# Optimization experiments

Hardware: AMD Instinct MI355X
Metric: run time of the kernel (lower is better)

Reference implementation:

```python
import jax, jax.numpy as jnp
import numpy as np

B, S, D = 4, 2048, 1024

def setup_inputs() -> dict:
    key = jax.random.key(0)
    k0, k1, k2, k3 = jax.random.split(key, 4)
    scale = 1.0 / np.sqrt(D)
    return {
        "x": jax.random.normal(k0, (B, S, D), dtype=jnp.float32),
        "Wq": jax.random.normal(k1, (D, D), dtype=jnp.float32) * scale,
        "Wk": jax.random.normal(k2, (D, D), dtype=jnp.float32) * scale,
        "Wv": jax.random.normal(k3, (D, D), dtype=jnp.float32) * scale,
    }

def reference(x, Wq, Wk, Wv):
    # x: [B,S,D]; Wq/Wk/Wv: [D_in, D_out] (equivalent to torch Linear weight transposed)
    q = jnp.einsum('bsd,de->bse', x, Wq)
    k = jnp.einsum('bsd,de->bse', x, Wk)
    v = jnp.einsum('bsd,de->bse', x, Wv)
    d_out = k.shape[-1]
    scores = jnp.einsum('bqe,bke->bqk', q, k)  # [B,S,S]
    S_ = scores.shape[-1]
    causal = jnp.tril(jnp.ones((S_, S_), dtype=bool))  # True = keep
    # masked_fill before scaling == after scaling (-inf invariant under positive scale)
    scores = jnp.where(causal, scores, -jnp.inf)
    attn = jax.nn.softmax(scores / jnp.sqrt(jnp.asarray(d_out, scores.dtype)), axis=-1)
    # dropout p=0.0 -> identity
    return jnp.einsum('bqk,bke->bqe', attn, v)
```

## Files before the change

kernel.cpp:

```cpp
#include <hip/hip_runtime.h>

#define B_  4
#define S_  2048
#define D_  1024
#define N_  (B_*S_)
#define SCALE 0.03125f
#define NEGINF (-3.0e38f)

typedef unsigned short u16;
typedef __attribute__((ext_vector_type(8))) short short8;
typedef __attribute__((ext_vector_type(4))) float floatx4;

__device__ __forceinline__ u16 f2bf(float f) {
    unsigned int u = __float_as_uint(f);
    u += 0x7FFFu + ((u >> 16) & 1u);
    return (u16)(u >> 16);
}
__device__ __forceinline__ float bf2f(u16 h) {
    return __uint_as_float((unsigned int)h << 16);
}

__device__ __forceinline__ void gl_lds16(const void* g, void* l) {
    __builtin_amdgcn_global_load_lds(
        (const __attribute__((address_space(1))) unsigned int*)g,
        (__attribute__((address_space(3))) unsigned int*)l, 16, 0, 0);
}

__device__ __forceinline__ int xcd_chunk(int bid, int nwg) {
    return (bid & 7) * (nwg >> 3) + (bid >> 3);
}

__global__ __launch_bounds__(256) void cast_fused(const float* __restrict__ x,
                                                  const float* __restrict__ Wq, const float* __restrict__ Wk,
                                                  const float* __restrict__ Wv,
                                                  u16* __restrict__ xb, u16* __restrict__ Wqb,
                                                  u16* __restrict__ Wkb, u16* __restrict__ Wvt) {
    __shared__ float t[32][33];
    const int blk = blockIdx.x;
    if (blk < 5120) {
        const float* src; u16* dst; size_t i;
        if (blk < 4096)      { src = x;  dst = xb;  i = (size_t)blk * 2048; }
        else if (blk < 4608) { src = Wq; dst = Wqb; i = (size_t)(blk - 4096) * 2048; }
        else                 { src = Wk; dst = Wkb; i = (size_t)(blk - 4608) * 2048; }
        i += (size_t)threadIdx.x * 8;
        float4 a = *(const float4*)&src[i];
        float4 b = *(const float4*)&src[i + 4];
        short8 o;
        o[0]=f2bf(a.x); o[1]=f2bf(a.y); o[2]=f2bf(a.z); o[3]=f2bf(a.w);
        o[4]=f2bf(b.x); o[5]=f2bf(b.y); o[6]=f2bf(b.z); o[7]=f2bf(b.w);
        *(short8*)&dst[i] = o;
    } else {
        const int tb = blk - 5120;
        const int c = threadIdx.x & 31, r0 = threadIdx.x >> 5;
        const int i0 = (tb >> 5) * 32, j0 = (tb & 31) * 32;
#pragma unroll
        for (int rr = 0; rr < 4; ++rr)
            t[r0 + rr * 8][c] = Wv[(size_t)(i0 + r0 + rr * 8) * D_ + j0 + c];
        __syncthreads();
#pragma unroll
        for (int rr = 0; rr < 4; ++rr)
            Wvt[(size_t)(j0 + r0 + rr * 8) * D_ + i0 + c] = f2bf(t[c][r0 + rr * 8]);
    }
}

__device__ __forceinline__ void mfma_nt_loop(const u16* __restrict__ A, int lda,
                                             const u16* __restrict__ Bp, int ldb,
                                             int m0, int n0, int kext,
                                             u16* As, u16* Bs, floatx4 acc[4][4])
{
    const int tid  = threadIdx.x;
    const int lane = tid & 63;
    const int lr   = lane & 15, quad = lane >> 4;
    const int wm   = ((tid >> 6) & 1) * 64, wn = (tid >> 7) * 64;
    const int e    = tid * 8;
    const int nt   = kext >> 6;

    auto stage = [&](int k0, int half) {
        u16* Ad = As + half * 8192;
        u16* Bd = Bs + half * 8192;
#pragma unroll
        for (int it = 0; it < 4; ++it) {
            int idx = it * 2048 + e;
            int row = idx >> 6;
            int cg  = (idx & 63) >> 3;
            int gc  = (cg ^ (row & 7)) << 3;
            gl_lds16(&A [(size_t)(m0 + row) * lda + k0 + gc], &Ad[idx]);
            gl_lds16(&Bp[(size_t)(n0 + row) * ldb + k0 + gc], &Bd[idx]);
        }
    };

    stage(0, 0);
    int cur = 0;
    for (int t = 0; t < nt; ++t) {
        if (t + 1 < nt) {
            stage((t + 1) << 6, cur ^ 1);
            asm volatile("s_waitcnt vmcnt(8)" ::: "memory");
        } else {
            asm volatile("s_waitcnt vmcnt(0)" ::: "memory");
        }
        __builtin_amdgcn_s_barrier();

        const u16* Asb = As + cur * 8192;
        const u16* Bsb = Bs + cur * 8192;
#pragma unroll
        for (int kk = 0; kk < 2; ++kk) {
            short8 af[4], bf[4];
            const int kg = kk * 4 + quad;
#pragma unroll
            for (int i = 0; i < 4; ++i) {
                int am = wm + i * 16 + lr;
                af[i] = *(const short8*)&Asb[am * 64 + ((kg ^ (am & 7)) << 3)];
                int bn = wn + i * 16 + lr;
                bf[i] = *(const short8*)&Bsb[bn * 64 + ((kg ^ (bn & 7)) << 3)];
            }
            __builtin_amdgcn_s_setprio(1);
#pragma unroll
            for (int i = 0; i < 4; ++i)
#pragma unroll
                for (int j = 0; j < 4; ++j)
                    acc[i][j] = __builtin_amdgcn_mfma_f32_16x16x32_bf16(af[i], bf[j], acc[i][j], 0, 0, 0);
            __builtin_amdgcn_s_setprio(0);
        }
        asm volatile("s_waitcnt lgkmcnt(0)" ::: "memory");
        __builtin_amdgcn_s_barrier();
        cur ^= 1;
    }
}

#define EPI_VARS                                              \
    const int lane = threadIdx.x & 63;                        \
    const int lr = lane & 15, quad = lane >> 4;               \
    const int wm = ((threadIdx.x >> 6) & 1) * 64, wn = (threadIdx.x >> 7) * 64;

__device__ __forceinline__ void mfma_nt_256(const u16* __restrict__ A, int lda,
                                            const u16* __restrict__ Bp, int ldb,
                                            int m0, int n0, int kext,
                                            u16* As, u16* Bs, floatx4 acc[8][4])
{
    const int tid  = threadIdx.x;
    const int lane = tid & 63;
    const int lr   = lane & 15, quad = lane >> 4;
    const int wid  = tid >> 6;
    const int wr   = wid >> 2;
    const int wc   = wid & 3;
    const int nt   = kext >> 6;

    auto stage2 = [&](int t, int c0) {
        const int k0 = t << 6;
        u16* Ad = As + (t & 1) * 16384;
        u16* Bd = Bs + (t & 1) * 16384;
#pragma unroll
        for (int c = c0; c < c0 + 2; ++c) {
            int idx = (c & 3) * 4096 + tid * 8;
            int row = idx >> 6;
            int cg  = (idx & 63) >> 3;
            int gc  = (cg ^ (row & 7)) << 3;
            if (c < 4) gl_lds16(&A [(size_t)(m0 + row) * lda + k0 + gc], &Ad[idx]);
            else       gl_lds16(&Bp[(size_t)(n0 + row) * ldb + k0 + gc], &Bd[idx]);
        }
    };

    stage2(0, 0); stage2(0, 2); stage2(0, 4); stage2(0, 6);

    for (int t = 0; t < nt; ++t) {
        const u16* Asb = As + (t & 1) * 16384;
        const u16* Bsb = Bs + (t & 1) * 16384;
        const bool pf = (t + 1 < nt);

        short8 af[4][2], bfA[2][2], bfB[2][2];

#pragma unroll
        for (int p = 0; p < 4; ++p) {
            if (p == 0) {
                if (pf) { stage2(t + 1, 0);
                          asm volatile("s_waitcnt vmcnt(2)" ::: "memory"); }
                else      asm volatile("s_waitcnt vmcnt(0)" ::: "memory");
                __builtin_amdgcn_s_barrier();
            } else if (pf) {
                stage2(t + 1, p * 2);
            }

            if (p == 0) {
#pragma unroll
                for (int i = 0; i < 4; ++i) {
                    int am = wr * 128 + i * 16 + lr;
#pragma unroll
                    for (int kk = 0; kk < 2; ++kk)
                        af[i][kk] = *(const short8*)&Asb[am * 64 + (((kk * 4 + quad) ^ (am & 7)) << 3)];
                }
#pragma unroll
                for (int j = 0; j < 2; ++j) {
                    int bn = wc * 64 + j * 16 + lr;
#pragma unroll
                    for (int kk = 0; kk < 2; ++kk)
                        bfA[j][kk] = *(const short8*)&Bsb[bn * 64 + (((kk * 4 + quad) ^ (bn & 7)) << 3)];
                }
            } else if (p == 1) {
#pragma unroll
                for (int j = 0; j < 2; ++j) {
                    int bn = wc * 64 + (j + 2) * 16 + lr;
#pragma unroll
                    for (int kk = 0; kk < 2; ++kk)
                        bfB[j][kk] = *(const short8*)&Bsb[bn * 64 + (((kk * 4 + quad) ^ (bn & 7)) << 3)];
                }
            } else if (p == 2) {
#pragma unroll
                for (int i = 0; i < 4; ++i) {
                    int am = wr * 128 + (i + 4) * 16 + lr;
#pragma unroll
                    for (int kk = 0; kk < 2; ++kk)
                        af[i][kk] = *(const short8*)&Asb[am * 64 + (((kk * 4 + quad) ^ (am & 7)) << 3)];
                }
            }

            const int mb = (p >> 1) * 4, nb = (p & 1) * 2;
            __builtin_amdgcn_s_setprio(1);
#pragma unroll
            for (int kk = 0; kk < 2; ++kk)
#pragma unroll
                for (int i = 0; i < 4; ++i)
#pragma unroll
                    for (int j = 0; j < 2; ++j)
                        acc[mb + i][nb + j] = __builtin_amdgcn_mfma_f32_16x16x32_bf16(
                            af[i][kk], (p & 1) ? bfB[j][kk] : bfA[j][kk], acc[mb + i][nb + j], 0, 0, 0);
            __builtin_amdgcn_s_setprio(0);
            asm volatile("s_waitcnt lgkmcnt(0)" ::: "memory");
            __builtin_amdgcn_s_barrier();
        }
    }
}

#define EPI256_VARS                                           \
    const int lane = threadIdx.x & 63;                        \
    const int lr = lane & 15, quad = lane >> 4;               \
    const int wr = (threadIdx.x >> 8) & 1, wc = (threadIdx.x >> 6) & 3;

__global__ __launch_bounds__(256) void mt_mfma(const u16* __restrict__ Wkb, const u16* __restrict__ Wqb,
                                               u16* __restrict__ Mt)
{
    __shared__ u16 As[16384], Bs[16384];
    const int m0 = blockIdx.y * 128, n0 = blockIdx.x * 128;
    floatx4 acc[4][4];
#pragma unroll
    for (int i = 0; i < 4; ++i)
#pragma unroll
        for (int j = 0; j < 4; ++j) acc[i][j] = (floatx4){0.f, 0.f, 0.f, 0.f};
    mfma_nt_loop(Wkb, D_, Wqb, D_, m0, n0, D_, As, Bs, acc);

    EPI_VARS
#pragma unroll
    for (int i = 0; i < 4; ++i)
#pragma unroll
        for (int j = 0; j < 4; ++j)
#pragma unroll
            for (int r = 0; r < 4; ++r)
                Mt[(size_t)(m0 + wm + i * 16 + quad * 4 + r) * D_ + n0 + wn + j * 16 + lr] = f2bf(acc[i][j][r]);
}

__global__ __launch_bounds__(512, 2) void yv_mfma(const u16* __restrict__ xb, const u16* __restrict__ Mt,
                                                  const u16* __restrict__ Wvt,
                                                  u16* __restrict__ Y, u16* __restrict__ Vt)
{
    __shared__ u16 As[32768], Bs[32768];
    const int lid = xcd_chunk(blockIdx.x, 256);
    floatx4 acc[8][4];
#pragma unroll
    for (int i = 0; i < 8; ++i)
#pragma unroll
        for (int j = 0; j < 4; ++j) acc[i][j] = (floatx4){0.f, 0.f, 0.f, 0.f};

    if (lid < 128) {
        const int m0 = (lid >> 2) * 256, n0 = (lid & 3) * 256;
        mfma_nt_256(xb, D_, Mt, D_, m0, n0, D_, As, Bs, acc);
        EPI256_VARS
#pragma unroll
        for (int i = 0; i < 8; ++i)
#pragma unroll
            for (int j = 0; j < 4; ++j)
#pragma unroll
                for (int r = 0; r < 4; ++r)
                    Y[(size_t)(m0 + wr * 128 + i * 16 + quad * 4 + r) * D_ + n0 + wc * 64 + j * 16 + lr]
                        = f2bf(acc[i][j][r]);
    } else {
        const int v = lid - 128;
        const int b = v >> 5;
        const int mloc = ((v >> 2) & 7) * 256;
        const int n0 = (v & 3) * 256;
        const int m0 = b * S_ + mloc;
        u16* Vb = Vt + (size_t)b * D_ * S_;
        mfma_nt_256(xb, D_, Wvt, D_, m0, n0, D_, As, Bs, acc);
        EPI256_VARS
#pragma unroll
        for (int i = 0; i < 8; ++i)
#pragma unroll
            for (int j = 0; j < 4; ++j) {
                const int ee = n0 + wc * 64 + j * 16 + lr;
                const int s4 = mloc + wr * 128 + i * 16 + quad * 4;
                ushort4 o;
                o.x = f2bf(acc[i][j][0]); o.y = f2bf(acc[i][j][1]);
                o.z = f2bf(acc[i][j][2]); o.w = f2bf(acc[i][j][3]);
                *(ushort4*)&Vb[(size_t)ee * S_ + s4] = o;
            }
    }
}

__global__ __launch_bounds__(512, 2) void scores_mfma(const u16* __restrict__ Y, const u16* __restrict__ xb,
                                                      u16* __restrict__ Sc)
{
    __shared__ u16 As[32768], Bs[32768];
    const int lid = xcd_chunk(blockIdx.x, 144);
    const int b = lid / 36;
    const int t = lid - b * 36;
    int qt = 0;
    while ((qt + 1) * (qt + 2) / 2 <= t) ++qt;
    const int kt = t - qt * (qt + 1) / 2;

    const u16* A  = Y  + (size_t)b * S_ * D_;
    const u16* Bp = xb + (size_t)b * S_ * D_;
    u16* Sb = Sc + (size_t)b * S_ * S_;
    const int m0 = qt * 256, n0 = kt * 256;
    floatx4 acc[8][4];
#pragma unroll
    for (int i = 0; i < 8; ++i)
#pragma unroll
        for (int j = 0; j < 4; ++j) acc[i][j] = (floatx4){0.f, 0.f, 0.f, 0.f};
    mfma_nt_256(A, D_, Bp, D_, m0, n0, D_, As, Bs, acc);

    EPI256_VARS
#pragma unroll
    for (int i = 0; i < 8; ++i)
#pragma unroll
        for (int r = 0; r < 4; ++r) {
            const int grow = m0 + wr * 128 + i * 16 + quad * 4 + r;
#pragma unroll
            for (int j = 0; j < 4; ++j) {
                const int gcol = n0 + wc * 64 + j * 16 + lr;
                const float v = (gcol <= grow) ? acc[i][j][r] * SCALE : NEGINF;
                Sb[(size_t)grow * S_ + gcol] = f2bf(v);
            }
        }
}

__global__ __launch_bounds__(256) void softmax_k(const u16* __restrict__ Sc, u16* __restrict__ P)
{
    const int row = blockIdx.x;
    const int b = row >> 11, q = row & (S_ - 1);
    const int L = ((q >> 7) + 1) << 7;
    const u16* rp = Sc + ((size_t)b * S_ + q) * S_;
    u16* pp = P + ((size_t)b * S_ + q) * S_;
    __shared__ float red[4];
    __shared__ float bc;
    const int tid = threadIdx.x;
    const int i = tid << 3;
    const bool act = i < L;

    float f[8];
    float lmax = -3.4e38f;
    if (act) {
        short8 v = *(const short8*)&rp[i];
#pragma unroll
        for (int k = 0; k < 8; ++k) { f[k] = bf2f((u16)v[k]); lmax = fmaxf(lmax, f[k]); }
    }
    for (int off = 32; off; off >>= 1) lmax = fmaxf(lmax, __shfl_down(lmax, off, 64));
    if ((tid & 63) == 0) red[tid >> 6] = lmax;
    __syncthreads();
    if (tid == 0) bc = fmaxf(fmaxf(red[0], red[1]), fmaxf(red[2], red[3]));
    __syncthreads();
    const float m = bc;

    float lsum = 0.f;
    if (act) {
#pragma unroll
        for (int k = 0; k < 8; ++k) { f[k] = __expf(f[k] - m); lsum += f[k]; }
    }
    for (int off = 32; off; off >>= 1) lsum += __shfl_down(lsum, off, 64);
    if ((tid & 63) == 0) red[tid >> 6] = lsum;
    __syncthreads();
    if (tid == 0) bc = red[0] + red[1] + red[2] + red[3];
    __syncthreads();
    const float inv = 1.0f / bc;

    if (act) {
        short8 o;
#pragma unroll
        for (int k = 0; k < 8; ++k) o[k] = (short)f2bf(f[k] * inv);
        *(short8*)&pp[i] = o;
    }
}

__global__ __launch_bounds__(256) void pv_mfma(const u16* __restrict__ P, const u16* __restrict__ Vt,
                                               float* __restrict__ O)
{
    const int lid = xcd_chunk(blockIdx.x, 512);
    const int b  = lid >> 7;
    const int r  = lid & 127;
    const int et = r >> 4, qt = r & 15;
    __shared__ u16 As[16384], Bs[16384];
    const u16* A  = P  + (size_t)b * S_ * S_;
    const u16* Bp = Vt + (size_t)b * D_ * S_;
    const int m0 = qt * 128, n0 = et * 128;
    const int kext = (qt + 1) * 128;
    floatx4 acc[4][4];
#pragma unroll
    for (int i = 0; i < 4; ++i)
#pragma unroll
        for (int j = 0; j < 4; ++j) acc[i][j] = (floatx4){0.f, 0.f, 0.f, 0.f};
    mfma_nt_loop(A, S_, Bp, S_, m0, n0, kext, As, Bs, acc);

    EPI_VARS
#pragma unroll
    for (int i = 0; i < 4; ++i)
#pragma unroll
        for (int r2 = 0; r2 < 4; ++r2) {
            const int grow = m0 + wm + i * 16 + quad * 4 + r2;
#pragma unroll
            for (int j = 0; j < 4; ++j)
                O[((size_t)b * S_ + grow) * D_ + n0 + wn + j * 16 + lr] = acc[i][j][r2];
        }
}

extern "C" void kernel_launch(void* const* d_in, const int* in_sizes, int n_in,
                              void* d_out, int out_size, void* d_ws, size_t ws_size,
                              hipStream_t stream) {
    const float* x  = (const float*)d_in[0];
    const float* Wq = (const float*)d_in[1];
    const float* Wk = (const float*)d_in[2];
    const float* Wv = (const float*)d_in[3];
    float* out = (float*)d_out;
    char* w = (char*)d_ws;

    u16* xb  = (u16*)(w);
    u16* Wqb = (u16*)(w + 16777216);
    u16* Wkb = (u16*)(w + 18874368);
    u16* Wvt = (u16*)(w + 20971520);
    u16* Mt  = (u16*)(w + 23068672);
    u16* Y   = (u16*)(w + 25165824);
    u16* Vt  = (u16*)(w + 41943040);
    u16* Sc  = (u16*)(w + 58720256);
    u16* P   = (u16*)(w + 92274688);

    cast_fused <<<dim3(6144),   256, 0, stream>>>(x, Wq, Wk, Wv, xb, Wqb, Wkb, Wvt);
    mt_mfma    <<<dim3(8, 8),   256, 0, stream>>>(Wkb, Wqb, Mt);
    yv_mfma    <<<dim3(256),    512, 0, stream>>>(xb, Mt, Wvt, Y, Vt);
    scores_mfma<<<dim3(144),    512, 0, stream>>>(Y, xb, Sc);
    softmax_k  <<<dim3(N_),     256, 0, stream>>>(Sc, P);
    pv_mfma    <<<dim3(512),    256, 0, stream>>>(P, Vt, out);
}
```

Measured before the change: 233.9 us.

## Restructure MFMA GEMM LDS layout into k-half slabs with finer-grained prefetch pipelining

Both the 128- and 256-tile NT GEMM mainloops now store LDS tiles as separate 32-wide k-half slabs with a 4-way XOR swizzle, in one unified shared buffer. Global-to-LDS prefetch of the next tile is split into smaller chunks interleaved between MFMA phases, with adjusted vmcnt waits. In the 256 kernel the wave mapping changes and B fragments are reused across two M halves, cutting LDS reads. The goal is better overlap of loads with MFMA and fewer bank conflicts, at the cost of more barriers per k-step.

Result: faster. 226.5 us (-3.2%).

```diff
diff --git a/kernel.cpp b/kernel.cpp
--- a/kernel.cpp
+++ b/kernel.cpp
@@ -63,56 +63,58 @@
     }
 }
 
-__device__ __forceinline__ void mfma_nt_loop(const u16* __restrict__ A, int lda,
-                                             const u16* __restrict__ Bp, int ldb,
-                                             int m0, int n0, int kext,
-                                             u16* As, u16* Bs, floatx4 acc[4][4])
+
+__device__ __forceinline__ void mfma_nt_128(const u16* __restrict__ A, int lda,
+                                            const u16* __restrict__ Bp, int ldb,
+                                            int m0, int n0, int kext,
+                                            u16* Sh, floatx4 acc[4][4])
 {
     const int tid  = threadIdx.x;
     const int lane = tid & 63;
     const int lr   = lane & 15, quad = lane >> 4;
     const int wm   = ((tid >> 6) & 1) * 64, wn = (tid >> 7) * 64;
-    const int e    = tid * 8;
     const int nt   = kext >> 6;
 
-    auto stage = [&](int k0, int half) {
-        u16* Ad = As + half * 8192;
-        u16* Bd = Bs + half * 8192;
-#pragma unroll
-        for (int it = 0; it < 4; ++it) {
-            int idx = it * 2048 + e;
-            int row = idx >> 6;
-            int cg  = (idx & 63) >> 3;
-            int gc  = (cg ^ (row & 7)) << 3;
-            gl_lds16(&A [(size_t)(m0 + row) * lda + k0 + gc], &Ad[idx]);
-            gl_lds16(&Bp[(size_t)(n0 + row) * ldb + k0 + gc], &Bd[idx]);
-        }
+    auto stage1 = [&](int t, int h) {
+        const int kk = h >> 2, mat = (h >> 1) & 1, half = h & 1;
+        const int idx = tid * 8;
+        const int row = half * 64 + (idx >> 5);
+        const int s   = (idx & 31) >> 3;
+        const int gk  = (t << 6) + kk * 32 + ((s ^ ((row >> 1) & 3)) << 3);
+        u16* dst = Sh + (t & 1) * 16384 + mat * 8192 + kk * 4096 + half * 2048 + idx;
+        const u16* src = mat ? &Bp[(size_t)(n0 + row) * ldb + gk]
+                             : &A [(size_t)(m0 + row) * lda + gk];
+        gl_lds16(src, dst);
     };
 
-    stage(0, 0);
-    int cur = 0;
+#pragma unroll
+    for (int h = 0; h < 8; ++h) stage1(0, h);
+
     for (int t = 0; t < nt; ++t) {
-        if (t + 1 < nt) {
-            stage((t + 1) << 6, cur ^ 1);
-            asm volatile("s_waitcnt vmcnt(8)" ::: "memory");
-        } else {
-            asm volatile("s_waitcnt vmcnt(0)" ::: "memory");
-        }
-        __builtin_amdgcn_s_barrier();
-
-        const u16* Asb = As + cur * 8192;
-        const u16* Bsb = Bs + cur * 8192;
-#pragma unroll
-        for (int kk = 0; kk < 2; ++kk) {
+        const u16* buf = Sh + (t & 1) * 16384;
+        const bool pf = (t + 1 < nt);
+#pragma unroll
+        for (int p = 0; p < 2; ++p) {
+            if (pf) {
+#pragma unroll
+                for (int h = 0; h < 4; ++h) stage1(t + 1, p * 4 + h);
+                asm volatile("s_waitcnt vmcnt(8)" ::: "memory");
+            } else if (p == 0) {
+                asm volatile("s_waitcnt vmcnt(4)" ::: "memory");
+            } else {
+                asm volatile("s_waitcnt vmcnt(0)" ::: "memory");
+            }
+            __builtin_amdgcn_s_barrier();
+
             short8 af[4], bf[4];
-            const int kg = kk * 4 + quad;
 #pragma unroll
             for (int i = 0; i < 4; ++i) {
-                int am = wm + i * 16 + lr;
-                af[i] = *(const short8*)&Asb[am * 64 + ((kg ^ (am & 7)) << 3)];
-                int bn = wn + i * 16 + lr;
-                bf[i] = *(const short8*)&Bsb[bn * 64 + ((kg ^ (bn & 7)) << 3)];
+                const int ar = wm + i * 16 + lr;
+                af[i] = *(const short8*)&buf[p * 4096 + ar * 32 + ((quad ^ ((ar >> 1) & 3)) << 3)];
+                const int br = wn + i * 16 + lr;
+                bf[i] = *(const short8*)&buf[8192 + p * 4096 + br * 32 + ((quad ^ ((br >> 1) & 3)) << 3)];
             }
+            asm volatile("s_waitcnt lgkmcnt(0)" ::: "memory");
             __builtin_amdgcn_s_setprio(1);
 #pragma unroll
             for (int i = 0; i < 4; ++i)
@@ -120,10 +122,8 @@
                 for (int j = 0; j < 4; ++j)
                     acc[i][j] = __builtin_amdgcn_mfma_f32_16x16x32_bf16(af[i], bf[j], acc[i][j], 0, 0, 0);
             __builtin_amdgcn_s_setprio(0);
-        }
-        asm volatile("s_waitcnt lgkmcnt(0)" ::: "memory");
-        __builtin_amdgcn_s_barrier();
-        cur ^= 1;
+            __builtin_amdgcn_s_barrier();
+        }
     }
 }
 
@@ -135,98 +135,109 @@
 __device__ __forceinline__ void mfma_nt_256(const u16* __restrict__ A, int lda,
                                             const u16* __restrict__ Bp, int ldb,
                                             int m0, int n0, int kext,
-                                            u16* As, u16* Bs, floatx4 acc[8][4])
+                                            u16* Sh, floatx4 acc[8][4])
 {
     const int tid  = threadIdx.x;
     const int lane = tid & 63;
     const int lr   = lane & 15, quad = lane >> 4;
-    const int wid  = tid >> 6;
-    const int wr   = wid >> 2;
-    const int wc   = wid & 3;
+    const int wr   = (tid >> 8) & 1, wc = (tid >> 6) & 3;
     const int nt   = kext >> 6;
 
-    auto stage2 = [&](int t, int c0) {
-        const int k0 = t << 6;
-        u16* Ad = As + (t & 1) * 16384;
-        u16* Bd = Bs + (t & 1) * 16384;
-#pragma unroll
-        for (int c = c0; c < c0 + 2; ++c) {
-            int idx = (c & 3) * 4096 + tid * 8;
-            int row = idx >> 6;
-            int cg  = (idx & 63) >> 3;
-            int gc  = (cg ^ (row & 7)) << 3;
-            if (c < 4) gl_lds16(&A [(size_t)(m0 + row) * lda + k0 + gc], &Ad[idx]);
-            else       gl_lds16(&Bp[(size_t)(n0 + row) * ldb + k0 + gc], &Bd[idx]);
-        }
+    auto stage1 = [&](int t, int h) {
+        const int kk = h >> 2, mat = (h >> 1) & 1, half = h & 1;
+        const int idx = tid * 8;
+        const int row = half * 128 + (idx >> 5);
+        const int s   = (idx & 31) >> 3;
+        const int gk  = (t << 6) + kk * 32 + ((s ^ ((row >> 1) & 3)) << 3);
+        u16* dst = Sh + (t & 1) * 32768 + mat * 16384 + kk * 8192 + half * 4096 + idx;
+        const u16* src = mat ? &Bp[(size_t)(n0 + row) * ldb + gk]
+                             : &A [(size_t)(m0 + row) * lda + gk];
+        gl_lds16(src, dst);
     };
 
-    stage2(0, 0); stage2(0, 2); stage2(0, 4); stage2(0, 6);
+#pragma unroll
+    for (int h = 0; h < 8; ++h) stage1(0, h);
 
     for (int t = 0; t < nt; ++t) {
-        const u16* Asb = As + (t & 1) * 16384;
-        const u16* Bsb = Bs + (t & 1) * 16384;
+        const u16* buf = Sh + (t & 1) * 32768;
         const bool pf = (t + 1 < nt);
-
-        short8 af[4][2], bfA[2][2], bfB[2][2];
-
-#pragma unroll
-        for (int p = 0; p < 4; ++p) {
-            if (p == 0) {
-                if (pf) { stage2(t + 1, 0);
-                          asm volatile("s_waitcnt vmcnt(2)" ::: "memory"); }
-                else      asm volatile("s_waitcnt vmcnt(0)" ::: "memory");
-                __builtin_amdgcn_s_barrier();
-            } else if (pf) {
-                stage2(t + 1, p * 2);
-            }
-
-            if (p == 0) {
-#pragma unroll
-                for (int i = 0; i < 4; ++i) {
-                    int am = wr * 128 + i * 16 + lr;
-#pragma unroll
-                    for (int kk = 0; kk < 2; ++kk)
-                        af[i][kk] = *(const short8*)&Asb[am * 64 + (((kk * 4 + quad) ^ (am & 7)) << 3)];
-                }
-#pragma unroll
-                for (int j = 0; j < 2; ++j) {
-                    int bn = wc * 64 + j * 16 + lr;
-#pragma unroll
-                    for (int kk = 0; kk < 2; ++kk)
-                        bfA[j][kk] = *(const short8*)&Bsb[bn * 64 + (((kk * 4 + quad) ^ (bn & 7)) << 3)];
-                }
-            } else if (p == 1) {
-#pragma unroll
-                for (int j = 0; j < 2; ++j) {
-                    int bn = wc * 64 + (j + 2) * 16 + lr;
-#pragma unroll
-                    for (int kk = 0; kk < 2; ++kk)
-                        bfB[j][kk] = *(const short8*)&Bsb[bn * 64 + (((kk * 4 + quad) ^ (bn & 7)) << 3)];
-                }
-            } else if (p == 2) {
-#pragma unroll
-                for (int i = 0; i < 4; ++i) {
-                    int am = wr * 128 + (i + 4) * 16 + lr;
-#pragma unroll
-                    for (int kk = 0; kk < 2; ++kk)
-                        af[i][kk] = *(const short8*)&Asb[am * 64 + (((kk * 4 + quad) ^ (am & 7)) << 3)];
-                }
-            }
-
-            const int mb = (p >> 1) * 4, nb = (p & 1) * 2;
-            __builtin_amdgcn_s_setprio(1);
-#pragma unroll
-            for (int kk = 0; kk < 2; ++kk)
-#pragma unroll
-                for (int i = 0; i < 4; ++i)
-#pragma unroll
-                    for (int j = 0; j < 2; ++j)
-                        acc[mb + i][nb + j] = __builtin_amdgcn_mfma_f32_16x16x32_bf16(
-                            af[i][kk], (p & 1) ? bfB[j][kk] : bfA[j][kk], acc[mb + i][nb + j], 0, 0, 0);
-            __builtin_amdgcn_s_setprio(0);
-            asm volatile("s_waitcnt lgkmcnt(0)" ::: "memory");
-            __builtin_amdgcn_s_barrier();
-        }
+        short8 af[4], bf[4];
+
+        if (pf) { stage1(t + 1, 0); stage1(t + 1, 1);
+                  asm volatile("s_waitcnt vmcnt(6)" ::: "memory"); }
+        else      asm volatile("s_waitcnt vmcnt(4)" ::: "memory");
+        __builtin_amdgcn_s_barrier();
+#pragma unroll
+        for (int i = 0; i < 4; ++i) {
+            const int ar = wr * 128 + i * 16 + lr;
+            af[i] = *(const short8*)&buf[ar * 32 + ((quad ^ ((ar >> 1) & 3)) << 3)];
+            const int br = wc * 64 + i * 16 + lr;
+            bf[i] = *(const short8*)&buf[16384 + br * 32 + ((quad ^ ((br >> 1) & 3)) << 3)];
+        }
+        asm volatile("s_waitcnt lgkmcnt(0)" ::: "memory");
+        __builtin_amdgcn_s_setprio(1);
+#pragma unroll
+        for (int i = 0; i < 4; ++i)
+#pragma unroll
+            for (int j = 0; j < 4; ++j)
+                acc[i][j] = __builtin_amdgcn_mfma_f32_16x16x32_bf16(af[i], bf[j], acc[i][j], 0, 0, 0);
+        __builtin_amdgcn_s_setprio(0);
+        __builtin_amdgcn_s_barrier();
+
+#pragma unroll
+        for (int i = 0; i < 4; ++i) {
+            const int ar = wr * 128 + 64 + i * 16 + lr;
+            af[i] = *(const short8*)&buf[ar * 32 + ((quad ^ ((ar >> 1) & 3)) << 3)];
+        }
+        if (pf) { stage1(t + 1, 2); stage1(t + 1, 3); }
+        __builtin_amdgcn_s_barrier();
+        asm volatile("s_waitcnt lgkmcnt(0)" ::: "memory");
+        __builtin_amdgcn_s_setprio(1);
+#pragma unroll
+        for (int i = 0; i < 4; ++i)
+#pragma unroll
+            for (int j = 0; j < 4; ++j)
+                acc[4 + i][j] = __builtin_amdgcn_mfma_f32_16x16x32_bf16(af[i], bf[j], acc[4 + i][j], 0, 0, 0);
+        __builtin_amdgcn_s_setprio(0);
+        __builtin_amdgcn_s_barrier();
+
+        if (pf) { stage1(t + 1, 4); stage1(t + 1, 5);
+                  asm volatile("s_waitcnt vmcnt(6)" ::: "memory"); }
+        else      asm volatile("s_waitcnt vmcnt(0)" ::: "memory");
+        __builtin_amdgcn_s_barrier();
+#pragma unroll
+        for (int i = 0; i < 4; ++i) {
+            const int ar = wr * 128 + i * 16 + lr;
+            af[i] = *(const short8*)&buf[8192 + ar * 32 + ((quad ^ ((ar >> 1) & 3)) << 3)];
+            const int br = wc * 64 + i * 16 + lr;
+            bf[i] = *(const short8*)&buf[24576 + br * 32 + ((quad ^ ((br >> 1) & 3)) << 3)];
+        }
+        asm volatile("s_waitcnt lgkmcnt(0)" ::: "memory");
+        __builtin_amdgcn_s_setprio(1);
+#pragma unroll
+        for (int i = 0; i < 4; ++i)
+#pragma unroll
+            for (int j = 0; j < 4; ++j)
+                acc[i][j] = __builtin_amdgcn_mfma_f32_16x16x32_bf16(af[i], bf[j], acc[i][j], 0, 0, 0);
+        __builtin_amdgcn_s_setprio(0);
+        __builtin_amdgcn_s_barrier();
+
+#pragma unroll
+        for (int i = 0; i < 4; ++i) {
+            const int ar = wr * 128 + 64 + i * 16 + lr;
+            af[i] = *(const short8*)&buf[8192 + ar * 32 + ((quad ^ ((ar >> 1) & 3)) << 3)];
+        }
+        if (pf) { stage1(t + 1, 6); stage1(t + 1, 7); }
+        __builtin_amdgcn_s_barrier();
+        asm volatile("s_waitcnt lgkmcnt(0)" ::: "memory");
+        __builtin_amdgcn_s_setprio(1);
+#pragma unroll
+        for (int i = 0; i < 4; ++i)
+#pragma unroll
+            for (int j = 0; j < 4; ++j)
+                acc[4 + i][j] = __builtin_amdgcn_mfma_f32_16x16x32_bf16(af[i], bf[j], acc[4 + i][j], 0, 0, 0);
+        __builtin_amdgcn_s_setprio(0);
+        __builtin_amdgcn_s_barrier();
     }
 }
 
@@ -238,14 +249,14 @@
 __global__ __launch_bounds__(256) void mt_mfma(const u16* __restrict__ Wkb, const u16* __restrict__ Wqb,
                                                u16* __restrict__ Mt)
 {
-    __shared__ u16 As[16384], Bs[16384];
+    __shared__ u16 Sh[32768];
     const int m0 = blockIdx.y * 128, n0 = blockIdx.x * 128;
     floatx4 acc[4][4];
 #pragma unroll
     for (int i = 0; i < 4; ++i)
 #pragma unroll
         for (int j = 0; j < 4; ++j) acc[i][j] = (floatx4){0.f, 0.f, 0.f, 0.f};
-    mfma_nt_loop(Wkb, D_, Wqb, D_, m0, n0, D_, As, Bs, acc);
+    mfma_nt_128(Wkb, D_, Wqb, D_, m0, n0, D_, Sh, acc);
 
     EPI_VARS
 #pragma unroll
@@ -261,7 +272,7 @@
                                                   const u16* __restrict__ Wvt,
                                                   u16* __restrict__ Y, u16* __restrict__ Vt)
 {
-    __shared__ u16 As[32768], Bs[32768];
+    __shared__ u16 Sh[65536];
     const int lid = xcd_chunk(blockIdx.x, 256);
     floatx4 acc[8][4];
 #pragma unroll
@@ -271,7 +282,7 @@
 
     if (lid < 128) {
         const int m0 = (lid >> 2) * 256, n0 = (lid & 3) * 256;
-        mfma_nt_256(xb, D_, Mt, D_, m0, n0, D_, As, Bs, acc);
+        mfma_nt_256(xb, D_, Mt, D_, m0, n0, D_, Sh, acc);
         EPI256_VARS
 #pragma unroll
         for (int i = 0; i < 8; ++i)
@@ -288,7 +299,7 @@
         const int n0 = (v & 3) * 256;
         const int m0 = b * S_ + mloc;
         u16* Vb = Vt + (size_t)b * D_ * S_;
-        mfma_nt_256(xb, D_, Wvt, D_, m0, n0, D_, As, Bs, acc);
+        mfma_nt_256(xb, D_, Wvt, D_, m0, n0, D_, Sh, acc);
         EPI256_VARS
 #pragma unroll
         for (int i = 0; i < 8; ++i)
@@ -307,7 +318,7 @@
 __global__ __launch_bounds__(512, 2) void scores_mfma(const u16* __restrict__ Y, const u16* __restrict__ xb,
                                                       u16* __restrict__ Sc)
 {
-    __shared__ u16 As[32768], Bs[32768];
+    __shared__ u16 Sh[65536];
     const int lid = xcd_chunk(blockIdx.x, 144);
     const int b = lid / 36;
     const int t = lid - b * 36;
@@ -324,7 +335,7 @@
     for (int i = 0; i < 8; ++i)
 #pragma unroll
         for (int j = 0; j < 4; ++j) acc[i][j] = (floatx4){0.f, 0.f, 0.f, 0.f};
-    mfma_nt_256(A, D_, Bp, D_, m0, n0, D_, As, Bs, acc);
+    mfma_nt_256(A, D_, Bp, D_, m0, n0, D_, Sh, acc);
 
     EPI256_VARS
 #pragma unroll
@@ -395,7 +406,7 @@
     const int b  = lid >> 7;
     const int r  = lid & 127;
     const int et = r >> 4, qt = r & 15;
-    __shared__ u16 As[16384], Bs[16384];
+    __shared__ u16 Sh[32768];
     const u16* A  = P  + (size_t)b * S_ * S_;
     const u16* Bp = Vt + (size_t)b * D_ * S_;
     const int m0 = qt * 128, n0 = et * 128;
@@ -405,7 +416,7 @@
     for (int i = 0; i < 4; ++i)
 #pragma unroll
         for (int j = 0; j < 4; ++j) acc[i][j] = (floatx4){0.f, 0.f, 0.f, 0.f};
-    mfma_nt_loop(A, S_, Bp, S_, m0, n0, kext, As, Bs, acc);
+    mfma_nt_128(A, S_, Bp, S_, m0, n0, kext, Sh, acc);
 
     EPI_VARS
 #pragma unroll
```
